# Kernel tuning notes

Measured on AMD Instinct MI355X. Metric: run time of the kernel, lower is better.

The kernel has to match this reference:

```python
import jax, jax.numpy as jnp
import numpy as np

D_MODEL = 1024
D_INNER = 2048  # d_model * expand_factor
EPS = 1e-6


def setup_inputs() -> dict:
    key = jax.random.key(0)
    ks = jax.random.split(key, 9)
    s_in = 1.0 / np.sqrt(D_MODEL)
    s_out = 1.0 / np.sqrt(D_INNER)
    x = jax.random.normal(ks[0], (4, 2048, D_MODEL), dtype=jnp.float32)
    # weights stored as [in, out] (transpose of nn.Linear layout)
    Wq = jax.random.uniform(ks[1], (D_MODEL, D_INNER), jnp.float32, -s_in, s_in)
    bq = jax.random.uniform(ks[2], (D_INNER,), jnp.float32, -s_in, s_in)
    Wk = jax.random.uniform(ks[3], (D_MODEL, D_INNER), jnp.float32, -s_in, s_in)
    bk = jax.random.uniform(ks[4], (D_INNER,), jnp.float32, -s_in, s_in)
    Wv = jax.random.uniform(ks[5], (D_MODEL, D_INNER), jnp.float32, -s_in, s_in)
    bv = jax.random.uniform(ks[6], (D_INNER,), jnp.float32, -s_in, s_in)
    Wo = jax.random.uniform(ks[7], (D_INNER, D_MODEL), jnp.float32, -s_out, s_out)
    bo = jax.random.uniform(ks[8], (D_MODEL,), jnp.float32, -s_out, s_out)
    return {"x": x, "Wq": Wq, "bq": bq, "Wk": Wk, "bk": bk,
            "Wv": Wv, "bv": bv, "Wo": Wo, "bo": bo}


def _phi(x):
    """ELU + 1 feature map (positive features)."""
    return jax.nn.elu(x) + 1.0


def reference(x, Wq, bq, Wk, bk, Wv, bv, Wo, bo):
    # x: [B, N, d_model]
    Q = _phi(x @ Wq + bq)          # [B, N, d_inner]
    K = _phi(x @ Wk + bk)          # [B, N, d_inner]
    V = x @ Wv + bv                # [B, N, d_inner]
    n = x.shape[1]
    # Causal linear attention; identical math to cumsum-of-outer-products:
    # numerator_n = sum_{m<=n} (Q_n . K_m) V_m ; denominator_n = sum_{m<=n} Q_n . K_m
    scores = jnp.einsum("bnd,bmd->bnm", Q, K)            # [B, N, N]
    mask = jnp.tril(jnp.ones((n, n), dtype=scores.dtype))
    scores = scores * mask
    numerator = jnp.einsum("bnm,bme->bne", scores, V)    # [B, N, d_inner]
    denominator = scores.sum(axis=-1, keepdims=True) + EPS
    out = numerator / denominator
    return out @ Wo + bo           # [B, N, d_model] (dropout is identity in eval)
```

## Files before the change

### kernel.cpp

```cpp
#include <hip/hip_runtime.h>
#include <hip/hip_bf16.h>


#define D_MODEL 1024
#define D_INNER 2048
#define SEQ     2048
#define NBATCH  4
#define MTOT    (NBATCH * SEQ)

typedef __attribute__((ext_vector_type(8))) __bf16 bf16x8;
typedef __attribute__((ext_vector_type(4))) float  f32x4;
typedef __attribute__((ext_vector_type(8))) short  short8v;
typedef __attribute__((ext_vector_type(4))) int    int4v;
typedef __attribute__((ext_vector_type(8))) int    int8v;

__device__ __forceinline__ short f2bf(float f) {
  union { float f; unsigned u; } x; x.f = f;
  unsigned r = x.u + 0x7fffu + ((x.u >> 16) & 1u);
  return (short)(r >> 16);
}
__device__ __forceinline__ float bf2f(short s) {
  union { unsigned u; float f; } x; x.u = ((unsigned)(unsigned short)s) << 16;
  return x.f;
}

__device__ __forceinline__ unsigned char f2fp8(float f) {
  union { float f; unsigned u; } x; x.f = f;
  const unsigned s = (x.u >> 24) & 0x80u;
  const unsigned a = x.u & 0x7fffffffu;
  if (a >= 0x43E00000u) return (unsigned char)(s | 0x7Eu);
  if (a < 0x3C800000u) {
    union { float f; unsigned u; } y; y.u = a;
    const int mi = (int)rintf(y.f * 512.0f);
    return (unsigned char)(s | (unsigned)mi);
  }
  const unsigned r = a + 0x7FFFFu + ((a >> 20) & 1u);
  const unsigned E = (r >> 23) - 120u;
  return (unsigned char)(s | (E << 3) | ((r >> 20) & 7u));
}

typedef const void __attribute__((address_space(1)))* as1cv;
typedef void __attribute__((address_space(3)))* as3v;

__device__ __forceinline__ void gload_lds16(const void* g, void* l) {
  __builtin_amdgcn_global_load_lds((as1cv)g, (as3v)l, 16, 0, 0);
}

__device__ __forceinline__ f32x4 mfma16(bf16x8 a, bf16x8 b, f32x4 c) {
  return __builtin_amdgcn_mfma_f32_16x16x32_bf16(a, b, c, 0, 0, 0);
}

__device__ __forceinline__ f32x4 mfma_fp8(int8v a, int8v b, f32x4 c) {
  asm("v_mfma_f32_16x16x128_f8f6f4 %0, %1, %2, %0"
      : "+v"(c) : "v"(a), "v"(b));
  return c;
}

__device__ __forceinline__ void gemm_pipe(const short* __restrict__ A, int lda, int aRowBase,
                                          const short* __restrict__ B, int ldb, int bRowBase,
                                          int k0, int k1, short* smem, f32x4 acc[4][4]) {
  const int t    = threadIdx.x;
  const int lane = t & 63, wid = t >> 6;
  const int wr = wid >> 1, wc = wid & 1;
  const int lrow = lane & 15, kblk = lane >> 4;

  const int r0 = t >> 2;
  const int sc = ((t & 3) ^ ((t >> 3) & 3)) * 8;
  const short* pA = A + (size_t)(aRowBase + r0) * lda + (k0 + sc);
  const short* pB = B + (size_t)(bRowBase + r0) * ldb + (k0 + sc);
  const size_t rA = (size_t)64 * lda;
  const size_t rB = (size_t)64 * ldb;

  int aoff[4], boff[4];
#pragma unroll
  for (int m = 0; m < 4; ++m) {
    const int row = wr * 64 + m * 16 + lrow;
    aoff[m] = (row * 64 + kblk * 16) ^ (((row >> 1) & 3) << 4);
  }
#pragma unroll
  for (int n = 0; n < 4; ++n) {
    const int row = wc * 64 + n * 16 + lrow;
    boff[n] = (row * 64 + kblk * 16) ^ (((row >> 1) & 3) << 4);
  }
  const char* cs = (const char*)smem;

#define STG(bufShorts) do {                                                    \
    gload_lds16(pA, smem + (bufShorts) + t * 8);                               \
    gload_lds16(pA + rA, smem + (bufShorts) + 2048 + t * 8);                   \
    gload_lds16(pB, smem + (bufShorts) + 4096 + t * 8);                        \
    gload_lds16(pB + rB, smem + (bufShorts) + 6144 + t * 8);                   \
    pA += 32; pB += 32;                                                        \
  } while (0)

#define CSTEP(bufBytes) do {                                                   \
    bf16x8 a[4], b[4];                                                         \
    _Pragma("unroll") for (int m = 0; m < 4; ++m)                              \
      a[m] = *(const bf16x8*)(cs + (bufBytes) + aoff[m]);                      \
    _Pragma("unroll") for (int n = 0; n < 4; ++n)                              \
      b[n] = *(const bf16x8*)(cs + (bufBytes) + 8192 + boff[n]);               \
    _Pragma("unroll") for (int m = 0; m < 4; ++m)                              \
      _Pragma("unroll") for (int n = 0; n < 4; ++n)                            \
        acc[m][n] = mfma16(a[m], b[n], acc[m][n]);                             \
  } while (0)

  STG(0);
  __syncthreads();
  for (int k = k0; k < k1; k += 64) {
    if (k + 32 < k1) STG(8192);
    CSTEP(0);
    __syncthreads();
    if (k + 64 < k1) STG(0);
    CSTEP(16384);
    __syncthreads();
  }
#undef STG
#undef CSTEP
}

__device__ __forceinline__ void gemm_pipe8(const unsigned char* __restrict__ A, int lda, int aRowBase,
                                           const unsigned char* __restrict__ B, int ldb, int bRowBase,
                                           int k0, int k1, char* smem, f32x4 acc[4][4]) {
  const int t    = threadIdx.x;
  const int lane = t & 63, wid = t >> 6;
  const int wr = wid >> 1, wc = wid & 1;
  const int lrow = lane & 15, kblk = lane >> 4;

  const int srow = t >> 3;
  const int scol = (((t & 7) ^ ((t >> 3) & 7)) << 4);
  const unsigned char* pA = A + (size_t)(aRowBase + srow) * lda + (k0 + scol);
  const unsigned char* pB = B + (size_t)(bRowBase + srow) * ldb + (k0 + scol);

  int aoff[4][2], boff[4][2];
#pragma unroll
  for (int m = 0; m < 4; ++m) {
    const int row = wr * 64 + m * 16 + lrow;
#pragma unroll
    for (int j = 0; j < 2; ++j)
      aoff[m][j] = row * 128 + (((kblk * 2 + j) ^ (row & 7)) << 4);
  }
#pragma unroll
  for (int n = 0; n < 4; ++n) {
    const int row = wc * 64 + n * 16 + lrow;
#pragma unroll
    for (int j = 0; j < 2; ++j)
      boff[n][j] = row * 128 + (((kblk * 2 + j) ^ (row & 7)) << 4);
  }

#define STG8(bufB) do {                                                        \
    _Pragma("unroll") for (int i = 0; i < 4; ++i) {                            \
      gload_lds16(pA + (size_t)(32 * i) * lda, smem + (bufB) + i * 4096 + t * 16);      \
      gload_lds16(pB + (size_t)(32 * i) * ldb, smem + (bufB) + 16384 + i * 4096 + t * 16); \
    }                                                                          \
    pA += 128; pB += 128;                                                      \
  } while (0)

#define CSTEP8(bufB) do {                                                      \
    int8v a[4], b[4];                                                          \
    _Pragma("unroll") for (int m = 0; m < 4; ++m)                              \
      _Pragma("unroll") for (int j = 0; j < 2; ++j)                            \
        ((int4v*)&a[m])[j] = *(const int4v*)(smem + (bufB) + aoff[m][j]);      \
    _Pragma("unroll") for (int n = 0; n < 4; ++n)                              \
      _Pragma("unroll") for (int j = 0; j < 2; ++j)                            \
        ((int4v*)&b[n])[j] = *(const int4v*)(smem + (bufB) + 16384 + boff[n][j]); \
    _Pragma("unroll") for (int m = 0; m < 4; ++m)                              \
      _Pragma("unroll") for (int n = 0; n < 4; ++n)                            \
        acc[m][n] = mfma_fp8(a[m], b[n], acc[m][n]);                           \
  } while (0)

  STG8(0);
  __syncthreads();
  for (int k = k0; k < k1; k += 256) {
    if (k + 128 < k1) STG8(32768);
    CSTEP8(0);
    __syncthreads();
    if (k + 256 < k1) STG8(0);
    CSTEP8(32768);
    __syncthreads();
  }
#undef STG8
#undef CSTEP8
}

__device__ __forceinline__ void gemm_pipe8s(const unsigned char* __restrict__ A, int lda, int aRowBase,
                                            const unsigned char* __restrict__ B, int ldb, int bRowBase,
                                            int k0, int k1, char* smem, f32x4 acc[4][4]) {
  const int t    = threadIdx.x;
  const int lane = t & 63, wid = t >> 6;
  const int wr = wid >> 1, wc = wid & 1;
  const int lrow = lane & 15, kblk = lane >> 4;

  const int srow = t >> 3;
  const int scol = (((t & 7) ^ ((t >> 3) & 7)) << 4);
  const unsigned char* pA = A + (size_t)(aRowBase + srow) * lda + (k0 + scol);
  const unsigned char* pB = B + (size_t)(bRowBase + srow) * ldb + (k0 + scol);

  int aoff[4][2], boff[4][2];
#pragma unroll
  for (int m = 0; m < 4; ++m) {
    const int row = wr * 64 + m * 16 + lrow;
#pragma unroll
    for (int j = 0; j < 2; ++j)
      aoff[m][j] = row * 128 + (((kblk * 2 + j) ^ (row & 7)) << 4);
  }
#pragma unroll
  for (int n = 0; n < 4; ++n) {
    const int row = wc * 64 + n * 16 + lrow;
#pragma unroll
    for (int j = 0; j < 2; ++j)
      boff[n][j] = row * 128 + (((kblk * 2 + j) ^ (row & 7)) << 4);
  }

  for (int k = k0; k < k1; k += 128) {
#pragma unroll
    for (int i = 0; i < 4; ++i) {
      gload_lds16(pA + (size_t)(32 * i) * lda, smem + i * 4096 + t * 16);
      gload_lds16(pB + (size_t)(32 * i) * ldb, smem + 16384 + i * 4096 + t * 16);
    }
    pA += 128; pB += 128;
    __syncthreads();
    int8v a[4], b[4];
#pragma unroll
    for (int m = 0; m < 4; ++m)
#pragma unroll
      for (int j = 0; j < 2; ++j)
        ((int4v*)&a[m])[j] = *(const int4v*)(smem + aoff[m][j]);
#pragma unroll
    for (int n = 0; n < 4; ++n)
#pragma unroll
      for (int j = 0; j < 2; ++j)
        ((int4v*)&b[n])[j] = *(const int4v*)(smem + 16384 + boff[n][j]);
#pragma unroll
    for (int m = 0; m < 4; ++m)
#pragma unroll
      for (int n = 0; n < 4; ++n)
        acc[m][n] = mfma_fp8(a[m], b[n], acc[m][n]);
    __syncthreads();
  }
}

#define GEMM_PRE                                           \
  __shared__ __align__(16) short smem[4 * 4096];           \
  f32x4 acc[4][4];                                         \
  _Pragma("unroll")                                        \
  for (int m = 0; m < 4; ++m)                              \
    _Pragma("unroll")                                      \
    for (int n = 0; n < 4; ++n) acc[m][n] = (f32x4){0.f, 0.f, 0.f, 0.f};

#define GEMM_PRE8                                          \
  __shared__ __align__(16) char smem8[65536];              \
  f32x4 acc[4][4];                                         \
  _Pragma("unroll")                                        \
  for (int m = 0; m < 4; ++m)                              \
    _Pragma("unroll")                                      \
    for (int n = 0; n < 4; ++n) acc[m][n] = (f32x4){0.f, 0.f, 0.f, 0.f};

#define GEMM_PRE8S                                         \
  __shared__ __align__(16) char smem8[32768];              \
  f32x4 acc[4][4];                                         \
  _Pragma("unroll")                                        \
  for (int m = 0; m < 4; ++m)                              \
    _Pragma("unroll")                                      \
    for (int n = 0; n < 4; ++n) acc[m][n] = (f32x4){0.f, 0.f, 0.f, 0.f};

#define EPILOG_VARS                                        \
  const int lane = threadIdx.x & 63;                       \
  const int wid  = threadIdx.x >> 6;                       \
  const int wr = wid >> 1, wc = wid & 1;                   \
  const int lrow = lane & 15, kblk = lane >> 4;

__device__ __forceinline__ void retile_store(const short* smem, short* dst0, int ldd) {
  const int er  = threadIdx.x >> 1;
  const int hf  = threadIdx.x & 1;
  short* dst = dst0 + (size_t)er * ldd + hf * 64;
#pragma unroll
  for (int i = 0; i < 8; ++i) {
    int byte = er * 256 + hf * 128 + i * 16;
    byte ^= (er & 7) << 5;
    ((short8v*)dst)[i] = *(const short8v*)((const char*)smem + byte);
  }
}

__global__ __launch_bounds__(256) void k_proj_qk8(const unsigned char* __restrict__ X8,
                                                  const unsigned char* __restrict__ WT8,
                                                  const float* __restrict__ bq,
                                                  const float* __restrict__ bk,
                                                  unsigned char* __restrict__ Qm8,
                                                  unsigned char* __restrict__ Km8) {
  GEMM_PRE8
  const int blockM = blockIdx.y * 128;
  const int blockN = blockIdx.x * 128;
  gemm_pipe8(X8, D_MODEL, blockM, WT8, D_MODEL, blockN, 0, D_MODEL, smem8, acc);
  EPILOG_VARS
  const int seg = blockN >> 11;
  const float* bias = (seg == 0) ? bq : bk;
  unsigned char* dst = (seg == 0) ? Qm8 : Km8;
#pragma unroll
  for (int m = 0; m < 4; ++m)
#pragma unroll
    for (int n = 0; n < 4; ++n) {
      const int e = (blockN & 2047) + wc * 64 + n * 16 + lrow;
      const float bvv = bias[e];
#pragma unroll
      for (int j = 0; j < 4; ++j) {
        const int row = blockM + wr * 64 + m * 16 + kblk * 4 + j;
        float v = acc[m][n][j] + bvv;
        v = (v > 0.f) ? (v + 1.f) : __expf(v);
        dst[(size_t)row * D_INNER + e] = f2fp8(v);
      }
    }
}

__global__ __launch_bounds__(256) void k_wfuse(const short* __restrict__ WvB,
                                               const short* __restrict__ WoT,
                                               short* __restrict__ wfT) {
  GEMM_PRE
  const int blockM = blockIdx.y * 128;
  const int blockN = blockIdx.x * 128;
  gemm_pipe(WvB, D_INNER, blockM, WoT, D_INNER, blockN, 0, D_INNER, smem, acc);
  EPILOG_VARS
#pragma unroll
  for (int m = 0; m < 4; ++m)
#pragma unroll
    for (int n = 0; n < 4; ++n) {
      const int cl = wc * 64 + n * 16 + lrow;
#pragma unroll
      for (int j = 0; j < 4; ++j) {
        const int rl = wr * 64 + m * 16 + kblk * 4 + j;
        int byte = cl * 256 + rl * 2;
        byte ^= (cl & 7) << 5;
        *(short*)((char*)smem + byte) = f2bf(acc[m][n][j]);
      }
    }
  __syncthreads();
  retile_store(smem, wfT + (size_t)blockN * D_MODEL + blockM, D_MODEL);
}

__global__ __launch_bounds__(256) void k_w2(const short* __restrict__ X,
                                            const short* __restrict__ WfT,
                                            const float* __restrict__ bfuse,
                                            short* __restrict__ w2T) {
  GEMM_PRE
  const int blockM = blockIdx.y * 128;
  const int blockN = blockIdx.x * 128;
  gemm_pipe(X, D_MODEL, blockM, WfT, D_MODEL, blockN, 0, D_MODEL, smem, acc);
  EPILOG_VARS
#pragma unroll
  for (int m = 0; m < 4; ++m)
#pragma unroll
    for (int n = 0; n < 4; ++n) {
      const int cl = wc * 64 + n * 16 + lrow;
      const float bvv = bfuse[blockN + cl];
#pragma unroll
      for (int j = 0; j < 4; ++j) {
        const int rl = wr * 64 + m * 16 + kblk * 4 + j;
        int byte = cl * 256 + rl * 2;
        byte ^= (cl & 7) << 5;
        *(short*)((char*)smem + byte) = f2bf(acc[m][n][j] + bvv);
      }
    }
  __syncthreads();
  const int b   = blockM >> 11;
  const int mm0 = blockM & 2047;
  retile_store(smem, w2T + ((size_t)b * D_MODEL + blockN) * SEQ + mm0, SEQ);
}

__global__ __launch_bounds__(256) void k_qkt8(const unsigned char* __restrict__ Q8,
                                              const unsigned char* __restrict__ K8,
                                              short* __restrict__ S,
                                              float* __restrict__ den_part) {
  const int b = blockIdx.y;
  const int t = blockIdx.x;
  int ib = (int)((-1.0f + sqrtf(8.0f * (float)t + 1.0f)) * 0.5f);
  while ((ib + 1) * (ib + 2) / 2 <= t) ++ib;
  while (ib * (ib + 1) / 2 > t) --ib;
  const int jb = t - ib * (ib + 1) / 2;
  GEMM_PRE8S
  short* Sb = S + (size_t)b * SEQ * SEQ;
  gemm_pipe8s(Q8 + (size_t)b * SEQ * D_INNER, D_INNER, ib * 128,
              K8 + (size_t)b * SEQ * D_INNER, D_INNER, jb * 128,
              0, D_INNER, smem8, acc);
  EPILOG_VARS
  const bool diag = (jb == ib);
  float sums[4][4];
#pragma unroll
  for (int m = 0; m < 4; ++m)
#pragma unroll
    for (int j = 0; j < 4; ++j) sums[m][j] = 0.f;
#pragma unroll
  for (int m = 0; m < 4; ++m)
#pragma unroll
    for (int n = 0; n < 4; ++n) {
      const int col = jb * 128 + wc * 64 + n * 16 + lrow;
#pragma unroll
      for (int j = 0; j < 4; ++j) {
        const int row = ib * 128 + wr * 64 + m * 16 + kblk * 4 + j;
        float v = acc[m][n][j];
        if (diag && col > row) v = 0.f;
        const short bs = f2bf(v);
        Sb[(size_t)row * SEQ + col] = bs;
        sums[m][j] += bf2f(bs);
      }
    }
#pragma unroll
  for (int m = 0; m < 4; ++m)
#pragma unroll
    for (int j = 0; j < 4; ++j) {
      float red = sums[m][j];
      red += __shfl_xor(red, 1, 64);
      red += __shfl_xor(red, 2, 64);
      red += __shfl_xor(red, 4, 64);
      red += __shfl_xor(red, 8, 64);
      if (lrow == 0) {
        const int rloc = wr * 64 + m * 16 + kblk * 4 + j;
        den_part[(size_t)(2 * jb + wc) * MTOT + b * SEQ + ib * 128 + rloc] = red;
      }
    }
}

__global__ __launch_bounds__(256) void k_sv(const short* __restrict__ S,
                                            const short* __restrict__ W2T,
                                            const float* __restrict__ den_part,
                                            const float* __restrict__ bo,
                                            float* __restrict__ out) {
  const int b = blockIdx.z;
  const int ib = 15 - blockIdx.y;
  const int eb = blockIdx.x;
  __shared__ float dnm[128];
  {
    const int t = threadIdx.x;
    if (t < 128) {
      float s = 1e-6f;
      const int nv = 2 * (ib + 1);
      const float* dp = den_part + b * SEQ + ib * 128 + t;
      for (int q = 0; q < nv; ++q) s += dp[(size_t)q * MTOT];
      dnm[t] = 1.0f / s;
    }
  }
  GEMM_PRE
  gemm_pipe(S + (size_t)b * SEQ * SEQ, SEQ, ib * 128,
            W2T + (size_t)b * (size_t)D_MODEL * SEQ, SEQ, eb * 128,
            0, (ib + 1) * 128, smem, acc);
  EPILOG_VARS
  const int blockM = ib * 128;
#pragma unroll
  for (int m = 0; m < 4; ++m)
#pragma unroll
    for (int j = 0; j < 4; ++j) {
      const int rloc = wr * 64 + m * 16 + kblk * 4 + j;
      const int row = blockM + rloc;
      const float rcp = dnm[rloc];
#pragma unroll
      for (int n = 0; n < 4; ++n) {
        const int col = eb * 128 + wc * 64 + n * 16 + lrow;
        out[((size_t)(b * SEQ + row)) * D_MODEL + col] = acc[m][n][j] * rcp + bo[col];
      }
    }
}

__global__ __launch_bounds__(256) void k_pre(const float* __restrict__ x,
                                             const float* __restrict__ Wq,
                                             const float* __restrict__ Wk,
                                             const float* __restrict__ Wv,
                                             const float* __restrict__ Wo,
                                             const float* __restrict__ bv,
                                             short* __restrict__ xb,
                                             unsigned char* __restrict__ x8,
                                             unsigned char* __restrict__ wqkT8,
                                             short* __restrict__ wvB,
                                             short* __restrict__ woT,
                                             float* __restrict__ bfuse) {
  __shared__ float tl[32][33];
  __shared__ float ws[4];
  const int bid = blockIdx.x;
  if (bid < 2048) {
    const int n4 = MTOT * D_MODEL / 4;
    int i = bid * 256 + threadIdx.x;
    const int stride = 2048 * 256;
    for (; i < n4; i += stride) {
      float4 v = ((const float4*)x)[i];
      short4 o;
      o.x = f2bf(v.x); o.y = f2bf(v.y); o.z = f2bf(v.z); o.w = f2bf(v.w);
      ((short4*)xb)[i] = o;
      uchar4 q;
      q.x = f2fp8(v.x); q.y = f2fp8(v.y); q.z = f2fp8(v.z); q.w = f2fp8(v.w);
      ((uchar4*)x8)[i] = q;
    }
  } else if (bid < 2048 + 4 * 2048) {
    const int z  = (bid - 2048) >> 11;
    const int bx = (bid - 2048) & 2047;
    const float* in = (z == 0) ? Wq : (z == 1) ? Wk : (z == 2) ? Wv : Wo;
    const int R = (z < 3) ? 1024 : 2048;
    const int C = (z < 3) ? 2048 : 1024;
    const int nbx = C >> 5;
    const int c0 = (bx % nbx) * 32, r0 = (bx / nbx) * 32;
    const int tx = threadIdx.x & 31, ty = (threadIdx.x >> 5) * 4;
    if (z == 2) {
#pragma unroll
      for (int i = 0; i < 4; ++i) {
        const size_t idx = (size_t)(r0 + ty + i) * C + (c0 + tx);
        wvB[idx] = f2bf(in[idx]);
      }
      return;
    }
#pragma unroll
    for (int i = 0; i < 4; ++i)
      tl[ty + i][tx] = in[(size_t)(r0 + ty + i) * C + (c0 + tx)];
    __syncthreads();
    if (z < 2) {
      unsigned char* o = wqkT8 + (size_t)z * D_INNER * D_MODEL;
#pragma unroll
      for (int i = 0; i < 4; ++i)
        o[(size_t)(c0 + ty + i) * R + (r0 + tx)] = f2fp8(tl[tx][ty + i]);
    } else {
#pragma unroll
      for (int i = 0; i < 4; ++i)
        woT[(size_t)(c0 + ty + i) * R + (r0 + tx)] = f2bf(tl[tx][ty + i]);
    }
  } else {
    const int o = bid - (2048 + 4 * 2048);
    const int t = threadIdx.x;
    float s = 0.f;
#pragma unroll
    for (int e = t; e < D_INNER; e += 256)
      s += bv[e] * Wo[(size_t)e * D_MODEL + o];
#pragma unroll
    for (int off = 32; off >= 1; off >>= 1) s += __shfl_down(s, off, 64);
    if ((t & 63) == 0) ws[t >> 6] = s;
    __syncthreads();
    if (t == 0) bfuse[o] = ws[0] + ws[1] + ws[2] + ws[3];
  }
}

extern "C" void kernel_launch(void* const* d_in, const int* in_sizes, int n_in,
                              void* d_out, int out_size, void* d_ws, size_t ws_size,
                              hipStream_t stream) {
  const float* x  = (const float*)d_in[0];
  const float* Wq = (const float*)d_in[1];
  const float* bq = (const float*)d_in[2];
  const float* Wk = (const float*)d_in[3];
  const float* bk = (const float*)d_in[4];
  const float* Wv = (const float*)d_in[5];
  const float* bv = (const float*)d_in[6];
  const float* Wo = (const float*)d_in[7];
  const float* bo = (const float*)d_in[8];
  float* out = (float*)d_out;

  short* xb    = (short*)d_ws;
  short* wvB   = xb    + (size_t)MTOT * D_MODEL;
  short* woT   = wvB   + (size_t)D_MODEL * D_INNER;
  short* wfT   = woT   + (size_t)D_MODEL * D_INNER;
  short* Sc    = wfT   + (size_t)D_MODEL * D_MODEL;
  short* w2T   = Sc    + (size_t)NBATCH * SEQ * SEQ;
  unsigned char* x8    = (unsigned char*)(w2T + (size_t)NBATCH * D_MODEL * SEQ);
  unsigned char* wqkT8 = x8    + (size_t)MTOT * D_MODEL;
  unsigned char* Qm8   = wqkT8 + (size_t)2 * D_INNER * D_MODEL;
  unsigned char* Km8   = Qm8   + (size_t)MTOT * D_INNER;
  float* den_part      = (float*)(Km8 + (size_t)MTOT * D_INNER);
  float* bfuse         = den_part + (size_t)32 * MTOT;

  dim3 b256(256);
  k_pre<<<11264, b256, 0, stream>>>(x, Wq, Wk, Wv, Wo, bv,
                                    xb, x8, wqkT8, wvB, woT, bfuse);
  k_wfuse<<<dim3(8, 8), b256, 0, stream>>>(wvB, woT, wfT);

  k_proj_qk8<<<dim3(32, 64), b256, 0, stream>>>(x8, wqkT8, bq, bk, Qm8, Km8);
  k_qkt8<<<dim3(136, NBATCH), b256, 0, stream>>>(Qm8, Km8, Sc, den_part);

  k_w2<<<dim3(8, 64), b256, 0, stream>>>(xb, wfT, bfuse, w2T);
  k_sv<<<dim3(8, 16, NBATCH), b256, 0, stream>>>(Sc, w2T, den_part, bo, out);
}
```

Measured before the change: 262.4 us.

## Merge independent GEMM kernels into combined launches to fill the GPU

Merges the weight-fusion GEMM (Wv·Wo, 64 blocks) into the Q/K projection launch, and the X·Wf GEMM (512 blocks) into the causal QK^T launch, dispatching on the block index. Independent work now runs concurrently instead of in small serial launches that underfill the device. This removes two kernel launches and their tail and launch gaps. The cost is that merged kernels reserve the larger shared memory footprint for every block, which can lower occupancy for the lighter path, and the mixed block durations can create load imbalance.

```diff
diff --git a/kernel.cpp b/kernel.cpp
--- a/kernel.cpp
+++ b/kernel.cpp
@@ -238,30 +238,13 @@
   }
 }
 
-#define GEMM_PRE                                           \
-  __shared__ __align__(16) short smem[4 * 4096];           \
+#define ACC_INIT                                           \
   f32x4 acc[4][4];                                         \
   _Pragma("unroll")                                        \
   for (int m = 0; m < 4; ++m)                              \
     _Pragma("unroll")                                      \
     for (int n = 0; n < 4; ++n) acc[m][n] = (f32x4){0.f, 0.f, 0.f, 0.f};
 
-#define GEMM_PRE8                                          \
-  __shared__ __align__(16) char smem8[65536];              \
-  f32x4 acc[4][4];                                         \
-  _Pragma("unroll")                                        \
-  for (int m = 0; m < 4; ++m)                              \
-    _Pragma("unroll")                                      \
-    for (int n = 0; n < 4; ++n) acc[m][n] = (f32x4){0.f, 0.f, 0.f, 0.f};
-
-#define GEMM_PRE8S                                         \
-  __shared__ __align__(16) char smem8[32768];              \
-  f32x4 acc[4][4];                                         \
-  _Pragma("unroll")                                        \
-  for (int m = 0; m < 4; ++m)                              \
-    _Pragma("unroll")                                      \
-    for (int n = 0; n < 4; ++n) acc[m][n] = (f32x4){0.f, 0.f, 0.f, 0.f};
-
 #define EPILOG_VARS                                        \
   const int lane = threadIdx.x & 63;                       \
   const int wid  = threadIdx.x >> 6;                       \
@@ -280,141 +263,149 @@
   }
 }
 
-__global__ __launch_bounds__(256) void k_proj_qk8(const unsigned char* __restrict__ X8,
-                                                  const unsigned char* __restrict__ WT8,
-                                                  const float* __restrict__ bq,
-                                                  const float* __restrict__ bk,
-                                                  unsigned char* __restrict__ Qm8,
-                                                  unsigned char* __restrict__ Km8) {
-  GEMM_PRE8
-  const int blockM = blockIdx.y * 128;
-  const int blockN = blockIdx.x * 128;
-  gemm_pipe8(X8, D_MODEL, blockM, WT8, D_MODEL, blockN, 0, D_MODEL, smem8, acc);
-  EPILOG_VARS
-  const int seg = blockN >> 11;
-  const float* bias = (seg == 0) ? bq : bk;
-  unsigned char* dst = (seg == 0) ? Qm8 : Km8;
-#pragma unroll
-  for (int m = 0; m < 4; ++m)
-#pragma unroll
-    for (int n = 0; n < 4; ++n) {
-      const int e = (blockN & 2047) + wc * 64 + n * 16 + lrow;
-      const float bvv = bias[e];
+__global__ __launch_bounds__(256) void k_projwf(const unsigned char* __restrict__ X8,
+                                                const unsigned char* __restrict__ WT8,
+                                                const float* __restrict__ bq,
+                                                const float* __restrict__ bk,
+                                                unsigned char* __restrict__ Qm8,
+                                                unsigned char* __restrict__ Km8,
+                                                const short* __restrict__ WvB,
+                                                const short* __restrict__ WoT,
+                                                short* __restrict__ wfT) {
+  __shared__ __align__(16) char smemb[65536];
+  ACC_INIT
+  const int bid = blockIdx.x;
+  if (bid < 2048) {
+    const int blockM = (bid >> 5) * 128;
+    const int blockN = (bid & 31) * 128;
+    gemm_pipe8(X8, D_MODEL, blockM, WT8, D_MODEL, blockN, 0, D_MODEL, smemb, acc);
+    EPILOG_VARS
+    const int seg = blockN >> 11;
+    const float* bias = (seg == 0) ? bq : bk;
+    unsigned char* dst = (seg == 0) ? Qm8 : Km8;
+#pragma unroll
+    for (int m = 0; m < 4; ++m)
+#pragma unroll
+      for (int n = 0; n < 4; ++n) {
+        const int e = (blockN & 2047) + wc * 64 + n * 16 + lrow;
+        const float bvv = bias[e];
+#pragma unroll
+        for (int j = 0; j < 4; ++j) {
+          const int row = blockM + wr * 64 + m * 16 + kblk * 4 + j;
+          float v = acc[m][n][j] + bvv;
+          v = (v > 0.f) ? (v + 1.f) : __expf(v);
+          dst[(size_t)row * D_INNER + e] = f2fp8(v);
+        }
+      }
+  } else {
+    short* smem = (short*)smemb;
+    const int bx = bid - 2048;
+    const int blockM = (bx >> 3) * 128;
+    const int blockN = (bx & 7) * 128;
+    gemm_pipe(WvB, D_INNER, blockM, WoT, D_INNER, blockN, 0, D_INNER, smem, acc);
+    EPILOG_VARS
+#pragma unroll
+    for (int m = 0; m < 4; ++m)
+#pragma unroll
+      for (int n = 0; n < 4; ++n) {
+        const int cl = wc * 64 + n * 16 + lrow;
+#pragma unroll
+        for (int j = 0; j < 4; ++j) {
+          const int rl = wr * 64 + m * 16 + kblk * 4 + j;
+          int byte = cl * 256 + rl * 2;
+          byte ^= (cl & 7) << 5;
+          *(short*)((char*)smem + byte) = f2bf(acc[m][n][j]);
+        }
+      }
+    __syncthreads();
+    retile_store(smem, wfT + (size_t)blockN * D_MODEL + blockM, D_MODEL);
+  }
+}
+
+__global__ __launch_bounds__(256) void k_qktw2(const unsigned char* __restrict__ Q8,
+                                               const unsigned char* __restrict__ K8,
+                                               short* __restrict__ S,
+                                               float* __restrict__ den_part,
+                                               const short* __restrict__ X,
+                                               const short* __restrict__ WfT,
+                                               const float* __restrict__ bfuse,
+                                               short* __restrict__ w2T) {
+  __shared__ __align__(16) char smemb[32768];
+  ACC_INIT
+  const int bid = blockIdx.x;
+  if (bid < 544) {
+    const int b = bid / 136;
+    const int t = bid - b * 136;
+    int ib = (int)((-1.0f + sqrtf(8.0f * (float)t + 1.0f)) * 0.5f);
+    while ((ib + 1) * (ib + 2) / 2 <= t) ++ib;
+    while (ib * (ib + 1) / 2 > t) --ib;
+    const int jb = t - ib * (ib + 1) / 2;
+    short* Sb = S + (size_t)b * SEQ * SEQ;
+    gemm_pipe8s(Q8 + (size_t)b * SEQ * D_INNER, D_INNER, ib * 128,
+                K8 + (size_t)b * SEQ * D_INNER, D_INNER, jb * 128,
+                0, D_INNER, smemb, acc);
+    EPILOG_VARS
+    const bool diag = (jb == ib);
+    float sums[4][4];
+#pragma unroll
+    for (int m = 0; m < 4; ++m)
+#pragma unroll
+      for (int j = 0; j < 4; ++j) sums[m][j] = 0.f;
+#pragma unroll
+    for (int m = 0; m < 4; ++m)
+#pragma unroll
+      for (int n = 0; n < 4; ++n) {
+        const int col = jb * 128 + wc * 64 + n * 16 + lrow;
+#pragma unroll
+        for (int j = 0; j < 4; ++j) {
+          const int row = ib * 128 + wr * 64 + m * 16 + kblk * 4 + j;
+          float v = acc[m][n][j];
+          if (diag && col > row) v = 0.f;
+          const short bs = f2bf(v);
+          Sb[(size_t)row * SEQ + col] = bs;
+          sums[m][j] += bf2f(bs);
+        }
+      }
+#pragma unroll
+    for (int m = 0; m < 4; ++m)
 #pragma unroll
       for (int j = 0; j < 4; ++j) {
-        const int row = blockM + wr * 64 + m * 16 + kblk * 4 + j;
-        float v = acc[m][n][j] + bvv;
-        v = (v > 0.f) ? (v + 1.f) : __expf(v);
-        dst[(size_t)row * D_INNER + e] = f2fp8(v);
-      }
-    }
-}
-
-__global__ __launch_bounds__(256) void k_wfuse(const short* __restrict__ WvB,
-                                               const short* __restrict__ WoT,
-                                               short* __restrict__ wfT) {
-  GEMM_PRE
-  const int blockM = blockIdx.y * 128;
-  const int blockN = blockIdx.x * 128;
-  gemm_pipe(WvB, D_INNER, blockM, WoT, D_INNER, blockN, 0, D_INNER, smem, acc);
-  EPILOG_VARS
-#pragma unroll
-  for (int m = 0; m < 4; ++m)
-#pragma unroll
-    for (int n = 0; n < 4; ++n) {
-      const int cl = wc * 64 + n * 16 + lrow;
-#pragma unroll
-      for (int j = 0; j < 4; ++j) {
-        const int rl = wr * 64 + m * 16 + kblk * 4 + j;
-        int byte = cl * 256 + rl * 2;
-        byte ^= (cl & 7) << 5;
-        *(short*)((char*)smem + byte) = f2bf(acc[m][n][j]);
-      }
-    }
-  __syncthreads();
-  retile_store(smem, wfT + (size_t)blockN * D_MODEL + blockM, D_MODEL);
-}
-
-__global__ __launch_bounds__(256) void k_w2(const short* __restrict__ X,
-                                            const short* __restrict__ WfT,
-                                            const float* __restrict__ bfuse,
-                                            short* __restrict__ w2T) {
-  GEMM_PRE
-  const int blockM = blockIdx.y * 128;
-  const int blockN = blockIdx.x * 128;
-  gemm_pipe(X, D_MODEL, blockM, WfT, D_MODEL, blockN, 0, D_MODEL, smem, acc);
-  EPILOG_VARS
-#pragma unroll
-  for (int m = 0; m < 4; ++m)
-#pragma unroll
-    for (int n = 0; n < 4; ++n) {
-      const int cl = wc * 64 + n * 16 + lrow;
-      const float bvv = bfuse[blockN + cl];
-#pragma unroll
-      for (int j = 0; j < 4; ++j) {
-        const int rl = wr * 64 + m * 16 + kblk * 4 + j;
-        int byte = cl * 256 + rl * 2;
-        byte ^= (cl & 7) << 5;
-        *(short*)((char*)smem + byte) = f2bf(acc[m][n][j] + bvv);
-      }
-    }
-  __syncthreads();
-  const int b   = blockM >> 11;
-  const int mm0 = blockM & 2047;
-  retile_store(smem, w2T + ((size_t)b * D_MODEL + blockN) * SEQ + mm0, SEQ);
-}
-
-__global__ __launch_bounds__(256) void k_qkt8(const unsigned char* __restrict__ Q8,
-                                              const unsigned char* __restrict__ K8,
-                                              short* __restrict__ S,
-                                              float* __restrict__ den_part) {
-  const int b = blockIdx.y;
-  const int t = blockIdx.x;
-  int ib = (int)((-1.0f + sqrtf(8.0f * (float)t + 1.0f)) * 0.5f);
-  while ((ib + 1) * (ib + 2) / 2 <= t) ++ib;
-  while (ib * (ib + 1) / 2 > t) --ib;
-  const int jb = t - ib * (ib + 1) / 2;
-  GEMM_PRE8S
-  short* Sb = S + (size_t)b * SEQ * SEQ;
-  gemm_pipe8s(Q8 + (size_t)b * SEQ * D_INNER, D_INNER, ib * 128,
-              K8 + (size_t)b * SEQ * D_INNER, D_INNER, jb * 128,
-              0, D_INNER, smem8, acc);
-  EPILOG_VARS
-  const bool diag = (jb == ib);
-  float sums[4][4];
-#pragma unroll
-  for (int m = 0; m < 4; ++m)
-#pragma unroll
-    for (int j = 0; j < 4; ++j) sums[m][j] = 0.f;
-#pragma unroll
-  for (int m = 0; m < 4; ++m)
-#pragma unroll
-    for (int n = 0; n < 4; ++n) {
-      const int col = jb * 128 + wc * 64 + n * 16 + lrow;
-#pragma unroll
-      for (int j = 0; j < 4; ++j) {
-        const int row = ib * 128 + wr * 64 + m * 16 + kblk * 4 + j;
-        float v = acc[m][n][j];
-        if (diag && col > row) v = 0.f;
-        const short bs = f2bf(v);
-        Sb[(size_t)row * SEQ + col] = bs;
-        sums[m][j] += bf2f(bs);
-      }
-    }
-#pragma unroll
-  for (int m = 0; m < 4; ++m)
-#pragma unroll
-    for (int j = 0; j < 4; ++j) {
-      float red = sums[m][j];
-      red += __shfl_xor(red, 1, 64);
-      red += __shfl_xor(red, 2, 64);
-      red += __shfl_xor(red, 4, 64);
-      red += __shfl_xor(red, 8, 64);
-      if (lrow == 0) {
-        const int rloc = wr * 64 + m * 16 + kblk * 4 + j;
-        den_part[(size_t)(2 * jb + wc) * MTOT + b * SEQ + ib * 128 + rloc] = red;
-      }
-    }
+        float red = sums[m][j];
+        red += __shfl_xor(red, 1, 64);
+        red += __shfl_xor(red, 2, 64);
+        red += __shfl_xor(red, 4, 64);
+        red += __shfl_xor(red, 8, 64);
+        if (lrow == 0) {
+          const int rloc = wr * 64 + m * 16 + kblk * 4 + j;
+          den_part[(size_t)(2 * jb + wc) * MTOT + b * SEQ + ib * 128 + rloc] = red;
+        }
+      }
+  } else {
+    short* smem = (short*)smemb;
+    const int bx = bid - 544;
+    const int blockM = (bx >> 3) * 128;
+    const int blockN = (bx & 7) * 128;
+    gemm_pipe(X, D_MODEL, blockM, WfT, D_MODEL, blockN, 0, D_MODEL, smem, acc);
+    EPILOG_VARS
+#pragma unroll
+    for (int m = 0; m < 4; ++m)
+#pragma unroll
+      for (int n = 0; n < 4; ++n) {
+        const int cl = wc * 64 + n * 16 + lrow;
+        const float bvv = bfuse[blockN + cl];
+#pragma unroll
+        for (int j = 0; j < 4; ++j) {
+          const int rl = wr * 64 + m * 16 + kblk * 4 + j;
+          int byte = cl * 256 + rl * 2;
+          byte ^= (cl & 7) << 5;
+          *(short*)((char*)smem + byte) = f2bf(acc[m][n][j] + bvv);
+        }
+      }
+    __syncthreads();
+    const int b   = blockM >> 11;
+    const int mm0 = blockM & 2047;
+    retile_store(smem, w2T + ((size_t)b * D_MODEL + blockN) * SEQ + mm0, SEQ);
+  }
 }
 
 __global__ __launch_bounds__(256) void k_sv(const short* __restrict__ S,
@@ -436,7 +427,8 @@
       dnm[t] = 1.0f / s;
     }
   }
-  GEMM_PRE
+  __shared__ __align__(16) short smem[4 * 4096];
+  ACC_INIT
   gemm_pipe(S + (size_t)b * SEQ * SEQ, SEQ, ib * 128,
             W2T + (size_t)b * (size_t)D_MODEL * SEQ, SEQ, eb * 128,
             0, (ib + 1) * 128, smem, acc);
@@ -561,11 +553,9 @@
   dim3 b256(256);
   k_pre<<<11264, b256, 0, stream>>>(x, Wq, Wk, Wv, Wo, bv,
                                     xb, x8, wqkT8, wvB, woT, bfuse);
-  k_wfuse<<<dim3(8, 8), b256, 0, stream>>>(wvB, woT, wfT);
-
-  k_proj_qk8<<<dim3(32, 64), b256, 0, stream>>>(x8, wqkT8, bq, bk, Qm8, Km8);
-  k_qkt8<<<dim3(136, NBATCH), b256, 0, stream>>>(Qm8, Km8, Sc, den_part);
-
-  k_w2<<<dim3(8, 64), b256, 0, stream>>>(xb, wfT, bfuse, w2T);
+  k_projwf<<<2112, b256, 0, stream>>>(x8, wqkT8, bq, bk, Qm8, Km8,
+                                      wvB, woT, wfT);
+  k_qktw2<<<1056, b256, 0, stream>>>(Qm8, Km8, Sc, den_part,
+                                     xb, wfT, bfuse, w2T);
   k_sv<<<dim3(8, 16, NBATCH), b256, 0, stream>>>(Sc, w2T, den_part, bo, out);
 }
```

Result: slower. 298.4 us (+13.7%).
